# Performance work log

Hardware: AMD Instinct MI355X
Metric: run time of the kernel (lower is better)

The kernel has to match this reference:

```python
import jax, jax.numpy as jnp
import numpy as np

DN = ('NCDHW', 'DHWIO', 'NCDHW')


def _w(key, cin, cout):
    # kernel_size=3 in 3D, Minkowski-style fan-in scaling, no bias
    scale = 1.0 / np.sqrt(cin * 27)
    return jax.random.normal(key, (3, 3, 3, cin, cout), dtype=jnp.float32) * scale


def setup_inputs() -> dict:
    key = jax.random.key(0)
    ks = jax.random.split(key, 7)
    x = jax.random.normal(ks[0], (1, 1024, 4, 4, 4), dtype=jnp.float32)
    chans = [(1024, 512), (512, 256), (256, 128), (128, 64), (64, 32), (32, 1)]
    ws = {f'w{i+1}': _w(ks[i + 1], ci, co) for i, (ci, co) in enumerate(chans)}
    return {'x': x, **ws}


def _ct(x, w, stride):
    # conv-transpose, kernel 3, SAME padding: stride 2 doubles resolution,
    # stride 1 preserves it (dense analog of Minkowski generative transpose conv)
    return jax.lax.conv_transpose(x, w, strides=(stride, stride, stride),
                                  padding='SAME', dimension_numbers=DN)


def reference(x, w1, w2, w3, w4, w5, w6):
    h = jax.nn.relu(_ct(x, w1, 2))   # 1024 -> 512, 4^3 -> 8^3
    h = jax.nn.relu(_ct(h, w2, 1))   # 512 -> 256
    h = jax.nn.relu(_ct(h, w3, 2))   # 256 -> 128, 8^3 -> 16^3
    h = jax.nn.relu(_ct(h, w4, 1))   # 128 -> 64
    h = jax.nn.relu(_ct(h, w5, 2))   # 64 -> 32, 16^3 -> 32^3
    return _ct(h, w6, 1)             # 32 -> 1, no final ReLU
```

## Files before the change

### kernel.cpp

```cpp
#include <hip/hip_runtime.h>

typedef _Float16 half8 __attribute__((ext_vector_type(8)));
typedef _Float16 half4v __attribute__((ext_vector_type(4)));
typedef float floatx4 __attribute__((ext_vector_type(4)));


__global__ __launch_bounds__(256) void pad_x_k(const float* __restrict__ X,
                                               _Float16* __restrict__ P) {
  int idx = blockIdx.x * 256 + threadIdx.x;
  if (idx >= 125 * 1024) return;
  int c = idx & 1023;
  int r = idx >> 10;
  int px = r % 5, py = (r / 5) % 5, pz = r / 25;
  float v = 0.f;
  if (px >= 1 && py >= 1 && pz >= 1)
    v = X[c * 64 + (pz - 1) * 16 + (py - 1) * 4 + (px - 1)];
  P[idx] = (_Float16)v;
}

template <int POS, int COUT, int S2IN, int NSPL, int PS>
__global__ __launch_bounds__(256) void red_k(const float* __restrict__ Pp,
                                             _Float16* __restrict__ P) {
  constexpr int C4 = COUT / 4;
  constexpr size_t U3 =
      S2IN ? (size_t)(POS / 2) * (POS / 2) * (POS / 2) : (size_t)POS * POS * POS;
  int idx = blockIdx.x * 256 + threadIdx.x;
  if (idx >= PS * PS * PS * C4) return;
  const int co = (idx % C4) * 4;
  const int r = idx / C4;
  const int px = r % PS, py = (r / PS) % PS, pz = r / (PS * PS);
  const int ix = px - 1, iy = py - 1, iz = pz - 1;
  float4 s = make_float4(0.f, 0.f, 0.f, 0.f);
  if ((unsigned)ix < (unsigned)POS && (unsigned)iy < (unsigned)POS &&
      (unsigned)iz < (unsigned)POS) {
    int j0, j1;
    size_t upos;
    if (S2IN) {
      const int pf[8] = {0, 8, 12, 16, 18, 22, 24, 26};
      const int tc[8] = {8, 4, 4, 2, 4, 2, 2, 1};
      const int cls = ((iz & 1) << 2) | ((iy & 1) << 1) | (ix & 1);
      j0 = pf[cls] * NSPL;
      j1 = j0 + tc[cls] * NSPL;
      constexpr int U = POS / 2;
      upos = ((size_t)(iz >> 1) * U + (iy >> 1)) * U + (ix >> 1);
    } else {
      j0 = 0;
      j1 = NSPL;
      upos = ((size_t)iz * POS + iy) * POS + ix;
    }
    const float* base = Pp + upos * COUT + co;
    for (int j = j0; j < j1; j++) {
      float4 v = *(const float4*)(base + (size_t)j * U3 * COUT);
      s.x += v.x; s.y += v.y; s.z += v.z; s.w += v.w;
    }
  }
  half4v h;
  h[0] = (_Float16)fmaxf(s.x, 0.f);
  h[1] = (_Float16)fmaxf(s.y, 0.f);
  h[2] = (_Float16)fmaxf(s.z, 0.f);
  h[3] = (_Float16)fmaxf(s.w, 0.f);
  *(half4v*)(P + (size_t)idx * 4) = h;
}

template <int CICHUNK, int CIN, int COUT, int NTILE, int TZ, int SOUTU,
          int PS, int SMODE, int TAPG, int STORE_MODE>
__global__ __launch_bounds__(256) void conv_mfma_k(
    const _Float16* __restrict__ P, const float* __restrict__ W,
    void* __restrict__ Optr) {
  constexpr int M = TZ * 16;
  constexpr bool S2 = (SMODE != 0);
  constexpr int MTZ = SOUTU / TZ;
  constexpr int MTXY = SOUTU / 4;
  constexpr int MT3 = MTZ * MTXY * MTXY;
  constexpr int KB = 32;
  constexpr int KP = 40;
  constexpr int KBI = CICHUNK / KB;
  constexpr int NCI = CIN / CICHUNK;
  constexpr int S = S2 ? 2 * SOUTU : SOUTU;
  constexpr int WM = (M == 128) ? 4 : 2;
  constexpr int NSUB = (WM == 4) ? (NTILE / 16) : (NTILE / 32);
  constexpr int BJ = KB * NTILE / 256;
  constexpr size_t U3 = (size_t)SOUTU * SOUTU * SOUTU;

  __shared__ __align__(16) _Float16 As[M][KP];
  __shared__ __align__(16) _Float16 Bs[NTILE][KP];

  int bx = blockIdx.x;
  int cls = 0, tap0 = 0, cig = blockIdx.z, jspl = 0;
  int p_toz = 0, p_toy = 0, p_tox = 0, p_wtap = 0;
  if (SMODE == 0) {
    const int tg = cig / NCI;
    cig -= tg * NCI;
    tap0 = tg * TAPG;
    jspl = blockIdx.z;
  } else if (SMODE == 1) {
    const int p = bx / MT3;
    bx -= p * MT3;
    jspl = p * NCI + cig;
    cls = (p >= 8) + (p >= 12) + (p >= 16) + (p >= 18) + (p >= 22) +
          (p >= 24) + (p >= 26);
    const int pf = cls == 0 ? 0 : cls == 1 ? 8 : cls == 2 ? 12
                 : cls == 3 ? 16 : cls == 4 ? 18 : cls == 5 ? 22
                 : cls == 6 ? 24 : 26;
    const int tl = p - pf;
    const int lz = (cls >> 2) & 1, ly = (cls >> 1) & 1, lx = cls & 1;
    const int shx = lx ? 0 : 1, shy = ly ? 0 : 1;
    const int iz = tl >> (shx + shy);
    const int rem = tl & ((1 << (shx + shy)) - 1);
    const int iy = rem >> shx;
    const int ix = rem & ((1 << shx) - 1);
    p_toz = lz ? 1 : iz;
    p_toy = ly ? 1 : iy;
    p_tox = lx ? 1 : ix;
    const int wz = lz ? 1 : 2 * iz, wy = ly ? 1 : 2 * iy,
              wx = lx ? 1 : 2 * ix;
    p_wtap = (wz * 3 + wy) * 3 + wx;
  } else {
    cls = bx / MT3;
    bx -= cls * MT3;
  }
  const int clz = (cls >> 2) & 1, cly = (cls >> 1) & 1, clx = cls & 1;

  const int u0z = (bx / (MTXY * MTXY)) * TZ;
  const int u0y = ((bx / MTXY) % MTXY) * 4;
  const int u0x = (bx % MTXY) * 4;
  const int n_base = blockIdx.y * NTILE;

  const int t = threadIdx.x;
  const int lane = t & 63;
  const int wave = t >> 6;

  const int skq = t & 3;
  const int sp = t >> 2;
  const int spx = sp & 3, spy = (sp >> 2) & 3, spz = sp >> 4;
  const int nB = t & (NTILE - 1);
  const int k0B = (t / NTILE) * BJ;
  const int m0w = (WM == 4) ? wave * 32 : (wave >> 1) * 32;
  const int n0w = (WM == 4) ? 0 : (wave & 1) * 32;
  const int fr = lane & 15;
  const int fq = lane >> 4;

  const int cz = S2 ? (clz ? 1 : 2) : 3;
  const int cy = S2 ? (cly ? 1 : 2) : 3;
  const int cx = S2 ? (clx ? 1 : 2) : 3;
  const int shx2 = clx ? 0 : 1, shy2 = cly ? 0 : 1;

  int NIT;
  if (SMODE == 0) NIT = TAPG * KBI;
  else if (SMODE == 1) NIT = KBI;
  else NIT = cz * cy * cx * KBI;

  floatx4 acc[2][NSUB];
#pragma unroll
  for (int i = 0; i < 2; i++)
#pragma unroll
    for (int s = 0; s < NSUB; s++) acc[i][s] = {0.f, 0.f, 0.f, 0.f};

  half8 rA0 = {}, rA1 = {}, nA0 = {}, nA1 = {};
  float rB[BJ] = {}, nBv[BJ] = {};

  auto load_it = [&](int it, half8& A0, half8& A1, float* BW) {
    int tap, kb;
    if (SMODE == 1) { tap = 0; kb = it; }
    else if (KBI == 1) { tap = it; kb = 0; }
    else { tap = it / KBI; kb = it - tap * KBI; }
    int toz, toy, tox, wtap;
    if (SMODE == 1) {
      toz = p_toz; toy = p_toy; tox = p_tox; wtap = p_wtap;
    } else if (SMODE == 0) {
      const int tt = tap0 + tap;
      const int iz = tt / 9;
      const int rem = tt - iz * 9;
      const int iy = rem / 3;
      const int ix = rem - iy * 3;
      toz = iz; toy = iy; tox = ix;
      wtap = tt;
    } else {
      const int iz = tap >> (shx2 + shy2);
      const int rem = tap & ((1 << (shx2 + shy2)) - 1);
      const int iy = rem >> shx2;
      const int ix = rem & ((1 << shx2) - 1);
      toz = clz ? 1 : iz; toy = cly ? 1 : iy; tox = clx ? 1 : ix;
      const int wz = clz ? 1 : 2 * iz, wy = cly ? 1 : 2 * iy,
                wx = clx ? 1 : 2 * ix;
      wtap = (wz * 3 + wy) * 3 + wx;
    }
    const int kof0 = cig * CICHUNK + kb * KB;
    const size_t pb =
        ((size_t)(((u0z + toz + spz) * PS + (u0y + toy + spy)) * PS +
                  (u0x + tox + spx))) * CIN + kof0 + skq * 8;
    A0 = *(const half8*)(P + pb);
    if (M == 128)
      A1 = *(const half8*)(P + pb + (size_t)4 * PS * PS * CIN);
    const float* wb =
        W + ((size_t)wtap * CIN + kof0 + k0B) * COUT + n_base + nB;
#pragma unroll
    for (int j = 0; j < BJ; j++) BW[j] = wb[(size_t)j * COUT];
  };

  load_it(0, rA0, rA1, rB);

  for (int it = 0; it < NIT; ++it) {
    *(half8*)&As[sp][skq * 8] = rA0;
    if (M == 128) *(half8*)&As[sp + 64][skq * 8] = rA1;
    if (BJ == 8) {
      half8 hb;
#pragma unroll
      for (int j = 0; j < 8; j++) hb[j] = (_Float16)rB[j];
      *(half8*)&Bs[nB][k0B] = hb;
    } else {
      half4v hb;
#pragma unroll
      for (int j = 0; j < 4; j++) hb[j] = (_Float16)rB[j];
      *(half4v*)&Bs[nB][k0B] = hb;
    }
    __syncthreads();
    if (it + 1 < NIT) load_it(it + 1, nA0, nA1, nBv);
    half8 a0 = *(const half8*)&As[m0w + fr][fq * 8];
    half8 a1 = *(const half8*)&As[m0w + 16 + fr][fq * 8];
#pragma unroll
    for (int s = 0; s < NSUB; s++) {
      half8 b = *(const half8*)&Bs[n0w + s * 16 + fr][fq * 8];
      acc[0][s] = __builtin_amdgcn_mfma_f32_16x16x32_f16(a0, b, acc[0][s], 0, 0, 0);
      acc[1][s] = __builtin_amdgcn_mfma_f32_16x16x32_f16(a1, b, acc[1][s], 0, 0, 0);
    }
    __syncthreads();
    rA0 = nA0;
    rA1 = nA1;
#pragma unroll
    for (int j = 0; j < BJ; j++) rB[j] = nBv[j];
  }

#pragma unroll
  for (int i = 0; i < 2; i++) {
#pragma unroll
    for (int r = 0; r < 4; r++) {
      const int m = m0w + i * 16 + fq * 4 + r;
      const int mz = m >> 4, my = (m >> 2) & 3, mx = m & 3;
      if (STORE_MODE == 2) {
        const int oz = 2 * (u0z + mz) + clz;
        const int oy = 2 * (u0y + my) + cly;
        const int ox = 2 * (u0x + mx) + clx;
        _Float16* o = (_Float16*)Optr +
            ((size_t)(((oz + 1) * (S + 2) + (oy + 1)) * (S + 2) + (ox + 1))) *
                COUT + n_base + n0w;
#pragma unroll
        for (int s = 0; s < NSUB; s++)
          o[s * 16 + fr] = (_Float16)fmaxf(acc[i][s][r], 0.f);
      } else {
        const size_t pos =
            ((size_t)((u0z + mz) * SOUTU + (u0y + my))) * SOUTU + (u0x + mx);
        float* o = (float*)Optr + ((size_t)jspl * U3 + pos) * COUT + n_base +
                   n0w;
#pragma unroll
        for (int s = 0; s < NSUB; s++) o[s * 16 + fr] = acc[i][s][r];
      }
    }
  }
}

__global__ __launch_bounds__(256) void conv6_k(const _Float16* __restrict__ P,
                                               const float* __restrict__ W6,
                                               float* __restrict__ O) {
  __shared__ __align__(16) float w[864];
  for (int i = threadIdx.x; i < 864; i += 256) w[i] = W6[i];
  __syncthreads();
  int idx = blockIdx.x * 256 + threadIdx.x;
  int x = idx & 31, y = (idx >> 5) & 31, z = idx >> 10;
  float a = 0.f;
  for (int dz = 0; dz < 3; dz++)
    for (int dy = 0; dy < 3; dy++)
      for (int dx = 0; dx < 3; dx++) {
        const _Float16* p =
            P + (size_t)(((z + dz) * 34 + (y + dy)) * 34 + (x + dx)) * 32;
        const float* ww = &w[((dz * 3 + dy) * 3 + dx) * 32];
#pragma unroll
        for (int c = 0; c < 32; c += 8) {
          half8 pv = *(const half8*)&p[c];
#pragma unroll
          for (int u = 0; u < 8; u++) a += (float)pv[u] * ww[c + u];
        }
      }
  O[idx] = a;
}

extern "C" void kernel_launch(void* const* d_in, const int* in_sizes, int n_in,
                              void* d_out, int out_size, void* d_ws,
                              size_t ws_size, hipStream_t stream) {
  const float* x  = (const float*)d_in[0];
  const float* w1 = (const float*)d_in[1];
  const float* w2 = (const float*)d_in[2];
  const float* w3 = (const float*)d_in[3];
  const float* w4 = (const float*)d_in[4];
  const float* w5 = (const float*)d_in[5];
  const float* w6 = (const float*)d_in[6];
  float* out = (float*)d_out;

  float* Q1 = (float*)d_ws;
  float* Q2 = Q1 + 3538944;
  float* Q3 = Q2 + 3145728;
  float* Q4 = Q3 + 3538944;
  _Float16* P1 = (_Float16*)(Q4 + 3145728);
  _Float16* P2 = P1 + 128000;
  _Float16* P3 = P2 + 512000;
  _Float16* P4 = P3 + 186624;
  _Float16* P5 = P4 + 746496;
  _Float16* P6 = P5 + 314432;

  hipMemsetAsync(P6, 0, 1257728 * sizeof(_Float16), stream);

  pad_x_k<<<500, 256, 0, stream>>>(x, P1);
  conv_mfma_k<256, 1024, 512, 64, 4, 4, 5, 1, 0, 3>
      <<<dim3(27, 8, 4), 256, 0, stream>>>(P1, w1, Q1);
  red_k<8, 512, 1, 4, 10><<<500, 256, 0, stream>>>(Q1, P2);
  conv_mfma_k<64, 512, 256, 64, 8, 8, 10, 0, 9, 3>
      <<<dim3(4, 4, 24), 256, 0, stream>>>(P2, w2, Q2);
  red_k<8, 256, 0, 24, 9><<<183, 256, 0, stream>>>(Q2, P3);
  conv_mfma_k<128, 256, 128, 64, 8, 8, 9, 1, 0, 3>
      <<<dim3(108, 2, 2), 256, 0, stream>>>(P3, w3, Q3);
  red_k<16, 128, 1, 2, 18><<<729, 256, 0, stream>>>(Q3, P4);
  conv_mfma_k<32, 128, 64, 64, 8, 16, 18, 0, 9, 3>
      <<<dim3(32, 1, 12), 256, 0, stream>>>(P4, w4, Q4);
  red_k<16, 64, 0, 12, 17><<<308, 256, 0, stream>>>(Q4, P5);
  conv_mfma_k<64, 64, 32, 32, 8, 16, 17, 2, 0, 2>
      <<<dim3(256, 1, 1), 256, 0, stream>>>(P5, w5, P6);
  conv6_k<<<128, 256, 0, stream>>>(P6, w6, out);

  (void)in_sizes; (void)n_in; (void)out_size; (void)ws_size;
}
```

Baseline: 204.8 us.

## Double-buffer LDS tiles, fuse input padding into first conv, shrink conv6 blocks

```diff
diff --git a/kernel.cpp b/kernel.cpp
--- a/kernel.cpp
+++ b/kernel.cpp
@@ -4,19 +4,6 @@
 typedef _Float16 half4v __attribute__((ext_vector_type(4)));
 typedef float floatx4 __attribute__((ext_vector_type(4)));
 
-
-__global__ __launch_bounds__(256) void pad_x_k(const float* __restrict__ X,
-                                               _Float16* __restrict__ P) {
-  int idx = blockIdx.x * 256 + threadIdx.x;
-  if (idx >= 125 * 1024) return;
-  int c = idx & 1023;
-  int r = idx >> 10;
-  int px = r % 5, py = (r / 5) % 5, pz = r / 25;
-  float v = 0.f;
-  if (px >= 1 && py >= 1 && pz >= 1)
-    v = X[c * 64 + (pz - 1) * 16 + (py - 1) * 4 + (px - 1)];
-  P[idx] = (_Float16)v;
-}
 
 template <int POS, int COUT, int S2IN, int NSPL, int PS>
 __global__ __launch_bounds__(256) void red_k(const float* __restrict__ Pp,
@@ -63,10 +50,10 @@
 }
 
 template <int CICHUNK, int CIN, int COUT, int NTILE, int TZ, int SOUTU,
-          int PS, int SMODE, int TAPG, int STORE_MODE>
+          int PS, int SMODE, int TAPG, int STORE_MODE, int GX>
 __global__ __launch_bounds__(256) void conv_mfma_k(
     const _Float16* __restrict__ P, const float* __restrict__ W,
-    void* __restrict__ Optr) {
+    void* __restrict__ Optr, const float* __restrict__ Xg) {
   constexpr int M = TZ * 16;
   constexpr bool S2 = (SMODE != 0);
   constexpr int MTZ = SOUTU / TZ;
@@ -82,8 +69,8 @@
   constexpr int BJ = KB * NTILE / 256;
   constexpr size_t U3 = (size_t)SOUTU * SOUTU * SOUTU;
 
-  __shared__ __align__(16) _Float16 As[M][KP];
-  __shared__ __align__(16) _Float16 Bs[NTILE][KP];
+  __shared__ __align__(16) _Float16 As[2][M][KP];
+  __shared__ __align__(16) _Float16 Bs[2][NTILE][KP];
 
   int bx = blockIdx.x;
   int cls = 0, tap0 = 0, cig = blockIdx.z, jspl = 0;
@@ -186,49 +173,73 @@
       wtap = (wz * 3 + wy) * 3 + wx;
     }
     const int kof0 = cig * CICHUNK + kb * KB;
-    const size_t pb =
-        ((size_t)(((u0z + toz + spz) * PS + (u0y + toy + spy)) * PS +
-                  (u0x + tox + spx))) * CIN + kof0 + skq * 8;
-    A0 = *(const half8*)(P + pb);
-    if (M == 128)
-      A1 = *(const half8*)(P + pb + (size_t)4 * PS * PS * CIN);
+    if (GX) {
+      const int gz = u0z + toz + spz - 1;
+      const int gy = u0y + toy + spy - 1;
+      const int gxx = u0x + tox + spx - 1;
+      const int c0 = kof0 + skq * 8;
+      if ((unsigned)gxx < (unsigned)SOUTU && (unsigned)gy < (unsigned)SOUTU &&
+          (unsigned)gz < (unsigned)SOUTU) {
+        const float* xb = Xg + (size_t)c0 * (SOUTU * SOUTU * SOUTU) +
+                          (gz * SOUTU + gy) * SOUTU + gxx;
+#pragma unroll
+        for (int u = 0; u < 8; u++)
+          A0[u] = (_Float16)xb[(size_t)u * (SOUTU * SOUTU * SOUTU)];
+      } else {
+#pragma unroll
+        for (int u = 0; u < 8; u++) A0[u] = (_Float16)0.f;
+      }
+    } else {
+      const size_t pb =
+          ((size_t)(((u0z + toz + spz) * PS + (u0y + toy + spy)) * PS +
+                    (u0x + tox + spx))) * CIN + kof0 + skq * 8;
+      A0 = *(const half8*)(P + pb);
+      if (M == 128)
+        A1 = *(const half8*)(P + pb + (size_t)4 * PS * PS * CIN);
+    }
     const float* wb =
         W + ((size_t)wtap * CIN + kof0 + k0B) * COUT + n_base + nB;
 #pragma unroll
     for (int j = 0; j < BJ; j++) BW[j] = wb[(size_t)j * COUT];
   };
 
-  load_it(0, rA0, rA1, rB);
-
-  for (int it = 0; it < NIT; ++it) {
-    *(half8*)&As[sp][skq * 8] = rA0;
-    if (M == 128) *(half8*)&As[sp + 64][skq * 8] = rA1;
+  auto stage = [&](int buf, half8& A0, half8& A1, float* BW) {
+    *(half8*)&As[buf][sp][skq * 8] = A0;
+    if (M == 128) *(half8*)&As[buf][sp + 64][skq * 8] = A1;
     if (BJ == 8) {
       half8 hb;
 #pragma unroll
-      for (int j = 0; j < 8; j++) hb[j] = (_Float16)rB[j];
-      *(half8*)&Bs[nB][k0B] = hb;
+      for (int j = 0; j < 8; j++) hb[j] = (_Float16)BW[j];
+      *(half8*)&Bs[buf][nB][k0B] = hb;
     } else {
       half4v hb;
 #pragma unroll
-      for (int j = 0; j < 4; j++) hb[j] = (_Float16)rB[j];
-      *(half4v*)&Bs[nB][k0B] = hb;
-    }
-    __syncthreads();
-    if (it + 1 < NIT) load_it(it + 1, nA0, nA1, nBv);
-    half8 a0 = *(const half8*)&As[m0w + fr][fq * 8];
-    half8 a1 = *(const half8*)&As[m0w + 16 + fr][fq * 8];
+      for (int j = 0; j < 4; j++) hb[j] = (_Float16)BW[j];
+      *(half4v*)&Bs[buf][nB][k0B] = hb;
+    }
+  };
+
+  load_it(0, rA0, rA1, rB);
+  stage(0, rA0, rA1, rB);
+  __syncthreads();
+
+  int cur = 0;
+  for (int it = 0; it < NIT; ++it) {
+    const bool more = (it + 1 < NIT);
+    if (more) load_it(it + 1, nA0, nA1, nBv);
+    half8 a0 = *(const half8*)&As[cur][m0w + fr][fq * 8];
+    half8 a1 = *(const half8*)&As[cur][m0w + 16 + fr][fq * 8];
 #pragma unroll
     for (int s = 0; s < NSUB; s++) {
-      half8 b = *(const half8*)&Bs[n0w + s * 16 + fr][fq * 8];
+      half8 b = *(const half8*)&Bs[cur][n0w + s * 16 + fr][fq * 8];
       acc[0][s] = __builtin_amdgcn_mfma_f32_16x16x32_f16(a0, b, acc[0][s], 0, 0, 0);
       acc[1][s] = __builtin_amdgcn_mfma_f32_16x16x32_f16(a1, b, acc[1][s], 0, 0, 0);
     }
-    __syncthreads();
-    rA0 = nA0;
-    rA1 = nA1;
-#pragma unroll
-    for (int j = 0; j < BJ; j++) rB[j] = nBv[j];
+    if (more) {
+      stage(cur ^ 1, nA0, nA1, nBv);
+      __syncthreads();
+    }
+    cur ^= 1;
   }
 
 #pragma unroll
@@ -259,13 +270,13 @@
   }
 }
 
-__global__ __launch_bounds__(256) void conv6_k(const _Float16* __restrict__ P,
+__global__ __launch_bounds__(128) void conv6_k(const _Float16* __restrict__ P,
                                                const float* __restrict__ W6,
                                                float* __restrict__ O) {
   __shared__ __align__(16) float w[864];
-  for (int i = threadIdx.x; i < 864; i += 256) w[i] = W6[i];
+  for (int i = threadIdx.x; i < 864; i += 128) w[i] = W6[i];
   __syncthreads();
-  int idx = blockIdx.x * 256 + threadIdx.x;
+  int idx = blockIdx.x * 128 + threadIdx.x;
   int x = idx & 31, y = (idx >> 5) & 31, z = idx >> 10;
   float a = 0.f;
   for (int dz = 0; dz < 3; dz++)
@@ -309,22 +320,21 @@
 
   hipMemsetAsync(P6, 0, 1257728 * sizeof(_Float16), stream);
 
-  pad_x_k<<<500, 256, 0, stream>>>(x, P1);
-  conv_mfma_k<256, 1024, 512, 64, 4, 4, 5, 1, 0, 3>
-      <<<dim3(27, 8, 4), 256, 0, stream>>>(P1, w1, Q1);
+  conv_mfma_k<256, 1024, 512, 64, 4, 4, 5, 1, 0, 3, 1>
+      <<<dim3(27, 8, 4), 256, 0, stream>>>(nullptr, w1, Q1, x);
   red_k<8, 512, 1, 4, 10><<<500, 256, 0, stream>>>(Q1, P2);
-  conv_mfma_k<64, 512, 256, 64, 8, 8, 10, 0, 9, 3>
-      <<<dim3(4, 4, 24), 256, 0, stream>>>(P2, w2, Q2);
+  conv_mfma_k<64, 512, 256, 64, 8, 8, 10, 0, 9, 3, 0>
+      <<<dim3(4, 4, 24), 256, 0, stream>>>(P2, w2, Q2, nullptr);
   red_k<8, 256, 0, 24, 9><<<183, 256, 0, stream>>>(Q2, P3);
-  conv_mfma_k<128, 256, 128, 64, 8, 8, 9, 1, 0, 3>
-      <<<dim3(108, 2, 2), 256, 0, stream>>>(P3, w3, Q3);
+  conv_mfma_k<128, 256, 128, 64, 8, 8, 9, 1, 0, 3, 0>
+      <<<dim3(108, 2, 2), 256, 0, stream>>>(P3, w3, Q3, nullptr);
   red_k<16, 128, 1, 2, 18><<<729, 256, 0, stream>>>(Q3, P4);
-  conv_mfma_k<32, 128, 64, 64, 8, 16, 18, 0, 9, 3>
-      <<<dim3(32, 1, 12), 256, 0, stream>>>(P4, w4, Q4);
+  conv_mfma_k<32, 128, 64, 64, 8, 16, 18, 0, 9, 3, 0>
+      <<<dim3(32, 1, 12), 256, 0, stream>>>(P4, w4, Q4, nullptr);
   red_k<16, 64, 0, 12, 17><<<308, 256, 0, stream>>>(Q4, P5);
-  conv_mfma_k<64, 64, 32, 32, 8, 16, 17, 2, 0, 2>
-      <<<dim3(256, 1, 1), 256, 0, stream>>>(P5, w5, P6);
-  conv6_k<<<128, 256, 0, stream>>>(P6, w6, out);
+  conv_mfma_k<64, 64, 32, 32, 8, 16, 17, 2, 0, 2, 0>
+      <<<dim3(256, 1, 1), 256, 0, stream>>>(P5, w5, P6, nullptr);
+  conv6_k<<<256, 128, 0, stream>>>(P6, w6, out);
 
   (void)in_sizes; (void)n_in; (void)out_size; (void)ws_size;
 }
```

New measurement: 208.0 us. Within noise of the previous version (+1.5%).
